# Kernel optimization log

Measured on AMD Instinct MI355X. Metric: run time of the kernel, lower is better.

## Reference

```python
import jax, jax.numpy as jnp
import numpy as np
import math

B, S, HID, H = 1, 2048, 1024, 16
D = HID // H  # head_dim = 64


def setup_inputs() -> dict:
    key = jax.random.key(0)
    ks = jax.random.split(key, 12)
    s = 0.02
    x = jax.random.normal(ks[0], (B, S, HID), jnp.float32)
    Wq = jax.random.normal(ks[1], (HID, HID), jnp.float32) * s
    bq = jnp.zeros((HID,), jnp.float32)
    Wk = jax.random.normal(ks[2], (HID, HID), jnp.float32) * s
    bk = jnp.zeros((HID,), jnp.float32)
    Wv = jax.random.normal(ks[3], (HID, HID), jnp.float32) * s
    bv = jnp.zeros((HID,), jnp.float32)
    Wo = jax.random.normal(ks[4], (HID, HID), jnp.float32) * s
    bo = jnp.zeros((HID,), jnp.float32)
    # nn.Parameter(torch.ones(3,3)) at init; small noise so the bias is non-degenerate
    cmw = jnp.ones((3, 3), jnp.float32) + 0.1 * jax.random.normal(ks[5], (3, 3), jnp.float32)
    # full causal [B,S,S] mask so the mask.shape[1]==seq_len branch is taken
    mask = jnp.tril(jnp.ones((B, S, S), jnp.int32))
    modality_info = jax.random.randint(ks[6], (B, S), 0, 3, dtype=jnp.int64)
    return dict(x=x, Wq=Wq, bq=bq, Wk=Wk, bk=bk, Wv=Wv, bv=bv, Wo=Wo, bo=bo,
                cmw=cmw, mask=mask, modality_info=modality_info)


def reference(x, Wq, bq, Wk, bk, Wv, bv, Wo, bo, cmw, mask, modality_info):
    b, s, _ = x.shape
    # QKV projections (torch Linear: y = x @ W.T + b), split into heads [B,H,S,D]
    q = (x @ Wq.T + bq).reshape(b, s, H, D).transpose(0, 2, 1, 3)
    k = (x @ Wk.T + bk).reshape(b, s, H, D).transpose(0, 2, 1, 3)
    v = (x @ Wv.T + bv).reshape(b, s, H, D).transpose(0, 2, 1, 3)
    scores = jnp.einsum('bhqd,bhkd->bhqk', q, k) / math.sqrt(D)  # [B,H,S,S]
    # cross-modal bias: gather from 3x3 table via pairwise modality indices -> [B,S,S]
    bias = cmw[modality_info[:, :, None], modality_info[:, None, :]]
    scores = scores + bias[:, None, :, :]  # equals original broadcast when B==1
    scores = jnp.where(mask[:, None, :, :] == 0, -1e9, scores)
    attn = jax.nn.softmax(scores, axis=-1)  # dropout is identity in eval
    ctx = jnp.einsum('bhqk,bhkd->bhqd', attn, v)          # [B,H,S,D]
    ctx = ctx.transpose(0, 2, 1, 3).reshape(b, s, HID)    # [B,S,HID]
    return ctx @ Wo.T + bo
```

## Files before the change

### kernel.cpp

```cpp
#include <hip/hip_runtime.h>
#include <hip/hip_bf16.h>
#include <math.h>

#define S_LEN 2048
#define HID   1024
#define NHEAD 16

using bf16x8 = __attribute__((ext_vector_type(8))) short;
using bf16x4 = __attribute__((ext_vector_type(4))) short;
using f32x4  = __attribute__((ext_vector_type(4))) float;

__device__ __forceinline__ float bf2f(short s) {
  union { unsigned u; float f; } c;
  c.u = ((unsigned)(unsigned short)s) << 16;
  return c.f;
}
__device__ __forceinline__ short f2bf(float f) {
  union { float f; unsigned u; } c; c.f = f;
  unsigned u = c.u;
  unsigned r = (u + 0x7fffu + ((u >> 16) & 1u)) >> 16;
  return (short)r;
}
__device__ __forceinline__ float loadf(const void* base, long idx, int is_bf) {
  return is_bf ? bf2f(((const short*)base)[idx]) : ((const float*)base)[idx];
}
__device__ __forceinline__ void gl_lds16(const void* g, void* l) {
  __builtin_amdgcn_global_load_lds(
      (const __attribute__((address_space(1))) void*)g,
      (__attribute__((address_space(3))) void*)l, 16, 0, 0);
}

__global__ void detect_kernel(const unsigned* __restrict__ xw,
                              const int* __restrict__ modw,
                              int* __restrict__ flags) {
  const int t = threadIdx.x;
  int cnt = 0;
  for (int i = t; i < 1024; i += 64) {
    const unsigned fld = (xw[i] >> 7) & 0xFFu;
    cnt += (fld >= 100u && fld <= 135u) ? 1 : 0;
  }
  int odd = 0;
  for (int i = 0; i < 4; ++i) {
    const int wv = modw[2 * (t + 64 * i) + 1];
    odd += (wv != 0) ? 1 : 0;
  }
  for (int m = 1; m < 64; m <<= 1) {
    cnt += __shfl_xor(cnt, m);
    odd += __shfl_xor(odd, m);
  }
  if (t == 0) {
    flags[0] = (cnt >= 512) ? 1 : 0;
    flags[1] = (odd == 0) ? 1 : 0;
  }
}

__global__ __launch_bounds__(256) void convert5(
    const void* __restrict__ s0, const void* __restrict__ s1, const void* __restrict__ s2,
    const void* __restrict__ s3, const void* __restrict__ s4,
    short* __restrict__ d0, short* __restrict__ d1, short* __restrict__ d2,
    short* __restrict__ d3, short* __restrict__ d4,
    const int* __restrict__ flags) {
  const int a = blockIdx.y;
  const void* src = (a == 0) ? s0 : (a == 1) ? s1 : (a == 2) ? s2 : (a == 3) ? s3 : s4;
  short* dst = (a == 0) ? d0 : (a == 1) ? d1 : (a == 2) ? d2 : (a == 3) ? d3 : d4;
  const long n = (a == 0) ? (2L << 20) : (1L << 20);
  const int is_bf = flags[0];
  long i = (long)(blockIdx.x * 256 + threadIdx.x) * 8;
  const long stride = (long)gridDim.x * 256 * 8;
  if (is_bf) {
    for (; i < n; i += stride)
      *(bf16x8*)(dst + i) = *(const bf16x8*)((const short*)src + i);
  } else {
    for (; i < n; i += stride) {
      const float* p = (const float*)src + i;
      bf16x8 r;
#pragma unroll
      for (int j = 0; j < 8; ++j) r[j] = f2bf(p[j]);
      *(bf16x8*)(dst + i) = r;
    }
  }
}

__global__ __launch_bounds__(256) void gemm_bt3(
    const short* __restrict__ A,
    const short* __restrict__ W0, const short* __restrict__ W1, const short* __restrict__ W2,
    const void* __restrict__ b0, const void* __restrict__ b1, const void* __restrict__ b2,
    void* __restrict__ C0, void* __restrict__ C1, void* __restrict__ C2,
    const int* __restrict__ flags, int nbn, int store_f32)
{
  constexpr int K = 1024;
  constexpr int N = 1024;
  __shared__ short As[128 * 32];
  __shared__ short Bs[64 * 32];

  const int t = threadIdx.x;
  const int w = t >> 6, lane = t & 63;
  const int l15 = lane & 15, quad = lane >> 4;
  const int wm = w >> 1, wn = w & 1;
  const int is_bf = flags[0];

  const int mat = blockIdx.x / nbn;
  const int n0 = (blockIdx.x % nbn) * 64;
  const int m0 = blockIdx.y * 128;

  const short* W  = (mat == 0) ? W0 : (mat == 1 ? W1 : W2);
  const void* bia = (mat == 0) ? b0 : (mat == 1 ? b1 : b2);
  void*       C   = (mat == 0) ? C0 : (mat == 1 ? C1 : C2);

  f32x4 acc[4][2];
  for (int mi = 0; mi < 4; ++mi)
    for (int ni = 0; ni < 2; ++ni)
      for (int r = 0; r < 4; ++r) acc[mi][ni][r] = 0.f;

  const int srow = t >> 2;
  const int sch  = (t & 3) * 8;
  const short* Ap = A + (long)(m0 + srow) * K + sch;
  const short* Wp = W + (long)(n0 + srow) * K + sch;
  short* AsW = &As[w * 512];
  short* BsW = &Bs[w * 512];

  for (int kt = 0; kt < K / 32; ++kt) {
    __syncthreads();
    gl_lds16(Ap + kt * 32, AsW);
    gl_lds16(Ap + kt * 32 + 64L * K, AsW + 2048);
    gl_lds16(Wp + kt * 32, BsW);
    __syncthreads();

    bf16x8 af[4], bfr[2];
    for (int mi = 0; mi < 4; ++mi)
      af[mi] = *(const bf16x8*)&As[(wm * 64 + mi * 16 + l15) * 32 + quad * 8];
    for (int ni = 0; ni < 2; ++ni)
      bfr[ni] = *(const bf16x8*)&Bs[(wn * 32 + ni * 16 + l15) * 32 + quad * 8];
    for (int mi = 0; mi < 4; ++mi)
      for (int ni = 0; ni < 2; ++ni)
        acc[mi][ni] = __builtin_amdgcn_mfma_f32_16x16x32_bf16(af[mi], bfr[ni], acc[mi][ni], 0, 0, 0);
  }

  for (int ni = 0; ni < 2; ++ni) {
    const int col = n0 + wn * 32 + ni * 16 + l15;
    const float bv = loadf(bia, col, is_bf);
    for (int mi = 0; mi < 4; ++mi) {
      const int row = m0 + wm * 64 + mi * 16 + quad * 4;
      for (int r = 0; r < 4; ++r) {
        const float v = acc[mi][ni][r] + bv;
        const long idx = (long)(row + r) * N + col;
        if (store_f32) ((float*)C)[idx] = v;
        else           ((short*)C)[idx] = f2bf(v);
      }
    }
  }
}

__global__ __launch_bounds__(256) void attn_split(
    const short* __restrict__ Q, const short* __restrict__ Kg, const short* __restrict__ Vg,
    const int* __restrict__ mod, const void* __restrict__ cmw,
    const int* __restrict__ flags,
    short* __restrict__ PO0, short* __restrict__ PO1,
    float* __restrict__ PL)
{
  __shared__ short Ks[64 * 80];
  __shared__ short Vt[64 * 80];
  __shared__ short Ps[4 * 16 * 80];
  __shared__ float cm[9];
  __shared__ int mods[2048];

  const int t = threadIdx.x;
  const int w = t >> 6, lane = t & 63;
  const int l15 = lane & 15, quad = lane >> 4;
  const int h = blockIdx.y;
  const int pair = blockIdx.x >> 1;
  const int par  = blockIdx.x & 1;
  const int m64 = flags[1];

  if (t < 9) cm[t] = loadf(cmw, t, flags[0]);
  for (int i = t; i < 2048; i += 256) mods[i] = mod[i << m64];
  __syncthreads();

  short* POp = (par == 0) ? PO0 : PO1;
  const int krow = t >> 3, kch = (t & 7) * 8;
  const int vkp = t & 63, vdc = (t >> 6) * 8;

  for (int si = 0; si < 2; ++si) {
    const int strip = (si == 0) ? pair : 31 - pair;
    const int q0 = strip * 64;
    const int nkt = strip + 1;

    const short* qb = Q + (long)(q0 + w * 16 + l15) * HID + h * 64 + quad * 8;
    const bf16x8 aq0 = *(const bf16x8*)qb;
    const bf16x8 aq1 = *(const bf16x8*)(qb + 32);

    int mrow[4];
    for (int r = 0; r < 4; ++r) mrow[r] = mods[q0 + w * 16 + quad * 4 + r];

    float lsum[4];
    f32x4 acc_o[4];
    for (int r = 0; r < 4; ++r) lsum[r] = 0.f;
    for (int ni = 0; ni < 4; ++ni)
      for (int r = 0; r < 4; ++r) acc_o[ni][r] = 0.f;

    bf16x8 rk0, rk1, rv0, rv1;
    if (par < nkt) {
      const long kb = (long)(par * 64) * HID + h * 64;
      rk0 = *(const bf16x8*)(Kg + kb + (long)krow * HID + kch);
      rk1 = *(const bf16x8*)(Kg + kb + (long)(krow + 32) * HID + kch);
      rv0 = *(const bf16x8*)(Vg + kb + (long)vkp * HID + vdc);
      rv1 = *(const bf16x8*)(Vg + kb + (long)vkp * HID + 32 + vdc);
    }

    for (int kt = par; kt < nkt; kt += 2) {
      __syncthreads();
      *(bf16x8*)&Ks[krow * 80 + kch] = rk0;
      *(bf16x8*)&Ks[(krow + 32) * 80 + kch] = rk1;
#pragma unroll
      for (int j = 0; j < 8; ++j) Vt[(vdc + j) * 80 + vkp] = rv0[j];
#pragma unroll
      for (int j = 0; j < 8; ++j) Vt[(vdc + 32 + j) * 80 + vkp] = rv1[j];
      __syncthreads();
      if (kt + 2 < nkt) {
        const long kb = (long)((kt + 2) * 64) * HID + h * 64;
        rk0 = *(const bf16x8*)(Kg + kb + (long)krow * HID + kch);
        rk1 = *(const bf16x8*)(Kg + kb + (long)(krow + 32) * HID + kch);
        rv0 = *(const bf16x8*)(Vg + kb + (long)vkp * HID + vdc);
        rv1 = *(const bf16x8*)(Vg + kb + (long)vkp * HID + 32 + vdc);
      }

      f32x4 sc[4];
      for (int nt = 0; nt < 4; ++nt) {
        const bf16x8 kb0 = *(const bf16x8*)&Ks[(nt * 16 + l15) * 80 + quad * 8];
        const bf16x8 kb1 = *(const bf16x8*)&Ks[(nt * 16 + l15) * 80 + 32 + quad * 8];
        f32x4 z;
        for (int r = 0; r < 4; ++r) z[r] = 0.f;
        z = __builtin_amdgcn_mfma_f32_16x16x32_bf16(aq0, kb0, z, 0, 0, 0);
        z = __builtin_amdgcn_mfma_f32_16x16x32_bf16(aq1, kb1, z, 0, 0, 0);
        sc[nt] = z;
      }

      float sv[4][4];
      for (int nt = 0; nt < 4; ++nt) {
        const int mcol = mods[kt * 64 + nt * 16 + l15];
        for (int r = 0; r < 4; ++r)
          sv[nt][r] = sc[nt][r] * 0.125f + cm[mrow[r] * 3 + mcol];
      }
      if (kt == nkt - 1) {
        for (int nt = 0; nt < 4; ++nt) {
          const int col = kt * 64 + nt * 16 + l15;
          for (int r = 0; r < 4; ++r) {
            const int row = q0 + w * 16 + quad * 4 + r;
            sv[nt][r] = (col <= row) ? sv[nt][r] : -1e30f;
          }
        }
      }
      short pb[4][4];
      for (int nt = 0; nt < 4; ++nt)
        for (int r = 0; r < 4; ++r) {
          const float p = __expf(fminf(sv[nt][r], 60.f));
          lsum[r] += p;
          pb[nt][r] = f2bf(p);
        }

      short* Pw = &Ps[w * 16 * 80];
      for (int nt = 0; nt < 4; ++nt)
        for (int r = 0; r < 4; ++r)
          Pw[(quad * 4 + r) * 80 + nt * 16 + l15] = pb[nt][r];
      asm volatile("s_waitcnt lgkmcnt(0)" ::: "memory");

      for (int kk = 0; kk < 2; ++kk) {
        const bf16x8 ap = *(const bf16x8*)&Pw[l15 * 80 + kk * 32 + quad * 8];
        for (int ni = 0; ni < 4; ++ni) {
          const bf16x8 bv = *(const bf16x8*)&Vt[(ni * 16 + l15) * 80 + kk * 32 + quad * 8];
          acc_o[ni] = __builtin_amdgcn_mfma_f32_16x16x32_bf16(ap, bv, acc_o[ni], 0, 0, 0);
        }
      }
    }

    for (int off = 1; off < 16; off <<= 1)
      for (int r = 0; r < 4; ++r) lsum[r] += __shfl_xor(lsum[r], off);

    for (int ni = 0; ni < 4; ++ni) {
      const int col = h * 64 + ni * 16 + l15;
      for (int r = 0; r < 4; ++r) {
        const int row = q0 + w * 16 + quad * 4 + r;
        POp[(long)row * HID + col] = f2bf(acc_o[ni][r]);
      }
    }
    if (l15 == 0) {
      for (int r = 0; r < 4; ++r) {
        const int row = q0 + w * 16 + quad * 4 + r;
        PL[par * 32768 + row * 16 + h] = lsum[r];
      }
    }
  }
}

__global__ __launch_bounds__(256) void attn_merge(
    const short* __restrict__ PO0, const short* __restrict__ PO1,
    const float* __restrict__ PL, short* __restrict__ CTX)
{
  const int row = blockIdx.x;
  const int t = threadIdx.x;
  const int h = t >> 4;
  const int d0 = (t & 15) * 4;
  const float l0 = PL[row * 16 + h], l1 = PL[32768 + row * 16 + h];
  const float inv = 1.f / (l0 + l1);
  const long b = (long)row * HID + h * 64 + d0;
  const bf16x4 o0 = *(const bf16x4*)&PO0[b];
  const bf16x4 o1 = *(const bf16x4*)&PO1[b];
  bf16x4 out;
#pragma unroll
  for (int j = 0; j < 4; ++j)
    out[j] = f2bf((bf2f(o0[j]) + bf2f(o1[j])) * inv);
  *(bf16x4*)&CTX[b] = out;
}

extern "C" void kernel_launch(void* const* d_in, const int* in_sizes, int n_in,
                              void* d_out, int out_size, void* d_ws, size_t ws_size,
                              hipStream_t stream) {
  constexpr long M1 = 1024L * 1024L;
  int*   flags = (int*)d_ws;
  short* base  = (short*)d_ws + 128;
  short* xb  = base;
  short* Wqb = xb + 2 * M1;
  short* Wkb = Wqb + M1;
  short* Wvb = Wkb + M1;
  short* Wob = Wvb + M1;
  short* Qw  = Wob + M1;
  short* Kw  = Qw + 2 * M1;
  short* Vw  = Kw + 2 * M1;
  short* CTX = Vw + 2 * M1;
  short* PO0 = CTX;
  short* PO1 = xb;
  float* PL  = (float*)Wvb;
  const int* modality = (const int*)d_in[11];

  detect_kernel<<<1, 64, 0, stream>>>((const unsigned*)d_in[0], modality, flags);
  convert5<<<dim3(512, 5), 256, 0, stream>>>(
      d_in[0], d_in[1], d_in[3], d_in[5], d_in[7],
      xb, Wqb, Wkb, Wvb, Wob, flags);

  gemm_bt3<<<dim3(48, 16), 256, 0, stream>>>(
      xb, Wqb, Wkb, Wvb, d_in[2], d_in[4], d_in[6],
      Qw, Kw, Vw, flags, 16, 0);
  attn_split<<<dim3(32, NHEAD), 256, 0, stream>>>(
      Qw, Kw, Vw, modality, d_in[9], flags, PO0, PO1, PL);
  attn_merge<<<dim3(S_LEN), 256, 0, stream>>>(PO0, PO1, PL, CTX);
  gemm_bt3<<<dim3(16, 16), 256, 0, stream>>>(
      CTX, Wob, Wob, Wob, d_in[8], d_in[8], d_in[8],
      d_out, d_out, d_out, flags, 16, 1);
}
```

Measured before the change: 183.2 us.

## Drop detect kernel, convert biases upfront, and double-buffer K/V tiles in attention

Removes the separate single-block detect kernel. Each conversion block now detects the dtype itself, and each attention block detects the int64 modality layout itself, which saves one launch and a serial dependency. Biases and the modality weight table are also converted to bf16 in the same conversion launch, so the GEMM epilogue and attention read them without a dtype branch. The attention inner loop now stages two K/V tiles per barrier pair into double-buffered LDS and prefetches the next two into registers. That halves the barrier count but raises register and LDS use, which may reduce occupancy.

```diff
diff --git a/kernel.cpp b/kernel.cpp
--- a/kernel.cpp
+++ b/kernel.cpp
@@ -21,72 +21,74 @@
   unsigned r = (u + 0x7fffu + ((u >> 16) & 1u)) >> 16;
   return (short)r;
 }
-__device__ __forceinline__ float loadf(const void* base, long idx, int is_bf) {
-  return is_bf ? bf2f(((const short*)base)[idx]) : ((const float*)base)[idx];
-}
 __device__ __forceinline__ void gl_lds16(const void* g, void* l) {
   __builtin_amdgcn_global_load_lds(
       (const __attribute__((address_space(1))) void*)g,
       (__attribute__((address_space(3))) void*)l, 16, 0, 0);
 }
-
-__global__ void detect_kernel(const unsigned* __restrict__ xw,
-                              const int* __restrict__ modw,
-                              int* __restrict__ flags) {
-  const int t = threadIdx.x;
+__device__ __forceinline__ int detect_bf(const unsigned* xw) {
   int cnt = 0;
-  for (int i = t; i < 1024; i += 64) {
+#pragma unroll
+  for (int i = 0; i < 64; ++i) {
     const unsigned fld = (xw[i] >> 7) & 0xFFu;
     cnt += (fld >= 100u && fld <= 135u) ? 1 : 0;
   }
-  int odd = 0;
-  for (int i = 0; i < 4; ++i) {
-    const int wv = modw[2 * (t + 64 * i) + 1];
-    odd += (wv != 0) ? 1 : 0;
-  }
-  for (int m = 1; m < 64; m <<= 1) {
-    cnt += __shfl_xor(cnt, m);
-    odd += __shfl_xor(odd, m);
-  }
-  if (t == 0) {
-    flags[0] = (cnt >= 512) ? 1 : 0;
-    flags[1] = (odd == 0) ? 1 : 0;
-  }
-}
-
-__global__ __launch_bounds__(256) void convert5(
+  return cnt >= 32;
+}
+
+__global__ __launch_bounds__(256) void convert10(
     const void* __restrict__ s0, const void* __restrict__ s1, const void* __restrict__ s2,
-    const void* __restrict__ s3, const void* __restrict__ s4,
+    const void* __restrict__ s3, const void* __restrict__ s4, const void* __restrict__ s5,
+    const void* __restrict__ s6, const void* __restrict__ s7, const void* __restrict__ s8,
+    const void* __restrict__ s9,
     short* __restrict__ d0, short* __restrict__ d1, short* __restrict__ d2,
-    short* __restrict__ d3, short* __restrict__ d4,
-    const int* __restrict__ flags) {
+    short* __restrict__ d3, short* __restrict__ d4, short* __restrict__ d5,
+    short* __restrict__ d6, short* __restrict__ d7, short* __restrict__ d8,
+    short* __restrict__ d9)
+{
+  const int is_bf = detect_bf((const unsigned*)s0);
   const int a = blockIdx.y;
-  const void* src = (a == 0) ? s0 : (a == 1) ? s1 : (a == 2) ? s2 : (a == 3) ? s3 : s4;
-  short* dst = (a == 0) ? d0 : (a == 1) ? d1 : (a == 2) ? d2 : (a == 3) ? d3 : d4;
-  const long n = (a == 0) ? (2L << 20) : (1L << 20);
-  const int is_bf = flags[0];
-  long i = (long)(blockIdx.x * 256 + threadIdx.x) * 8;
-  const long stride = (long)gridDim.x * 256 * 8;
-  if (is_bf) {
+  const void* src; short* dst; long n;
+  if      (a == 0) { src = s0; dst = d0; n = 2L << 20; }
+  else if (a == 1) { src = s1; dst = d1; n = 1L << 20; }
+  else if (a == 2) { src = s2; dst = d2; n = 1L << 20; }
+  else if (a == 3) { src = s3; dst = d3; n = 1L << 20; }
+  else if (a == 4) { src = s4; dst = d4; n = 1L << 20; }
+  else if (a == 5) { src = s5; dst = d5; n = 1024; }
+  else if (a == 6) { src = s6; dst = d6; n = 1024; }
+  else if (a == 7) { src = s7; dst = d7; n = 1024; }
+  else if (a == 8) { src = s8; dst = d8; n = 1024; }
+  else             { src = s9; dst = d9; n = 9; }
+
+  if (n >= 1024) {
+    long i = (long)(blockIdx.x * 256 + threadIdx.x) * 8;
+    const long stride = (long)gridDim.x * 256 * 8;
+    if (is_bf) {
+      for (; i < n; i += stride)
+        *(bf16x8*)(dst + i) = *(const bf16x8*)((const short*)src + i);
+    } else {
+      for (; i < n; i += stride) {
+        const float* p = (const float*)src + i;
+        bf16x8 r;
+#pragma unroll
+        for (int j = 0; j < 8; ++j) r[j] = f2bf(p[j]);
+        *(bf16x8*)(dst + i) = r;
+      }
+    }
+  } else {
+    long i = blockIdx.x * 256 + threadIdx.x;
+    const long stride = (long)gridDim.x * 256;
     for (; i < n; i += stride)
-      *(bf16x8*)(dst + i) = *(const bf16x8*)((const short*)src + i);
-  } else {
-    for (; i < n; i += stride) {
-      const float* p = (const float*)src + i;
-      bf16x8 r;
-#pragma unroll
-      for (int j = 0; j < 8; ++j) r[j] = f2bf(p[j]);
-      *(bf16x8*)(dst + i) = r;
-    }
+      dst[i] = is_bf ? ((const short*)src)[i] : f2bf(((const float*)src)[i]);
   }
 }
 
 __global__ __launch_bounds__(256) void gemm_bt3(
     const short* __restrict__ A,
     const short* __restrict__ W0, const short* __restrict__ W1, const short* __restrict__ W2,
-    const void* __restrict__ b0, const void* __restrict__ b1, const void* __restrict__ b2,
+    const short* __restrict__ b0, const short* __restrict__ b1, const short* __restrict__ b2,
     void* __restrict__ C0, void* __restrict__ C1, void* __restrict__ C2,
-    const int* __restrict__ flags, int nbn, int store_f32)
+    int nbn, int store_f32)
 {
   constexpr int K = 1024;
   constexpr int N = 1024;
@@ -97,14 +99,13 @@
   const int w = t >> 6, lane = t & 63;
   const int l15 = lane & 15, quad = lane >> 4;
   const int wm = w >> 1, wn = w & 1;
-  const int is_bf = flags[0];
 
   const int mat = blockIdx.x / nbn;
   const int n0 = (blockIdx.x % nbn) * 64;
   const int m0 = blockIdx.y * 128;
 
   const short* W  = (mat == 0) ? W0 : (mat == 1 ? W1 : W2);
-  const void* bia = (mat == 0) ? b0 : (mat == 1 ? b1 : b2);
+  const short* bia = (mat == 0) ? b0 : (mat == 1 ? b1 : b2);
   void*       C   = (mat == 0) ? C0 : (mat == 1 ? C1 : C2);
 
   f32x4 acc[4][2];
@@ -138,7 +139,7 @@
 
   for (int ni = 0; ni < 2; ++ni) {
     const int col = n0 + wn * 32 + ni * 16 + l15;
-    const float bv = loadf(bia, col, is_bf);
+    const float bv = bf2f(bia[col]);
     for (int mi = 0; mi < 4; ++mi) {
       const int row = m0 + wm * 64 + mi * 16 + quad * 4;
       for (int r = 0; r < 4; ++r) {
@@ -153,13 +154,12 @@
 
 __global__ __launch_bounds__(256) void attn_split(
     const short* __restrict__ Q, const short* __restrict__ Kg, const short* __restrict__ Vg,
-    const int* __restrict__ mod, const void* __restrict__ cmw,
-    const int* __restrict__ flags,
+    const int* __restrict__ mod, const short* __restrict__ cmw,
     short* __restrict__ PO0, short* __restrict__ PO1,
     float* __restrict__ PL)
 {
-  __shared__ short Ks[64 * 80];
-  __shared__ short Vt[64 * 80];
+  __shared__ short Ks[2][64 * 80];
+  __shared__ short Vt[2][64 * 80];
   __shared__ short Ps[4 * 16 * 80];
   __shared__ float cm[9];
   __shared__ int mods[2048];
@@ -170,13 +170,18 @@
   const int h = blockIdx.y;
   const int pair = blockIdx.x >> 1;
   const int par  = blockIdx.x & 1;
-  const int m64 = flags[1];
-
-  if (t < 9) cm[t] = loadf(cmw, t, flags[0]);
+
+  int oddbits = 0;
+#pragma unroll
+  for (int i = 0; i < 64; ++i) oddbits |= mod[2 * i + 1];
+  const int m64 = (oddbits == 0) ? 1 : 0;
+
+  if (t < 9) cm[t] = bf2f(cmw[t]);
   for (int i = t; i < 2048; i += 256) mods[i] = mod[i << m64];
   __syncthreads();
 
   short* POp = (par == 0) ? PO0 : PO1;
+  short* Pw = &Ps[w * 16 * 80];
   const int krow = t >> 3, kch = (t & 7) * 8;
   const int vkp = t & 63, vdc = (t >> 6) * 8;
 
@@ -198,52 +203,42 @@
     for (int ni = 0; ni < 4; ++ni)
       for (int r = 0; r < 4; ++r) acc_o[ni][r] = 0.f;
 
-    bf16x8 rk0, rk1, rv0, rv1;
-    if (par < nkt) {
-      const long kb = (long)(par * 64) * HID + h * 64;
-      rk0 = *(const bf16x8*)(Kg + kb + (long)krow * HID + kch);
-      rk1 = *(const bf16x8*)(Kg + kb + (long)(krow + 32) * HID + kch);
-      rv0 = *(const bf16x8*)(Vg + kb + (long)vkp * HID + vdc);
-      rv1 = *(const bf16x8*)(Vg + kb + (long)vkp * HID + 32 + vdc);
-    }
-
-    for (int kt = par; kt < nkt; kt += 2) {
-      __syncthreads();
-      *(bf16x8*)&Ks[krow * 80 + kch] = rk0;
-      *(bf16x8*)&Ks[(krow + 32) * 80 + kch] = rk1;
-#pragma unroll
-      for (int j = 0; j < 8; ++j) Vt[(vdc + j) * 80 + vkp] = rv0[j];
-#pragma unroll
-      for (int j = 0; j < 8; ++j) Vt[(vdc + 32 + j) * 80 + vkp] = rv1[j];
-      __syncthreads();
-      if (kt + 2 < nkt) {
-        const long kb = (long)((kt + 2) * 64) * HID + h * 64;
-        rk0 = *(const bf16x8*)(Kg + kb + (long)krow * HID + kch);
-        rk1 = *(const bf16x8*)(Kg + kb + (long)(krow + 32) * HID + kch);
-        rv0 = *(const bf16x8*)(Vg + kb + (long)vkp * HID + vdc);
-        rv1 = *(const bf16x8*)(Vg + kb + (long)vkp * HID + 32 + vdc);
-      }
-
+    bf16x8 rkA[2], rvA[2], rkB[2], rvB[2];
+    auto ldtile = [&](int kt_, bf16x8* rk, bf16x8* rv) {
+      const long kb = (long)(kt_ * 64) * HID + h * 64;
+      rk[0] = *(const bf16x8*)(Kg + kb + (long)krow * HID + kch);
+      rk[1] = *(const bf16x8*)(Kg + kb + (long)(krow + 32) * HID + kch);
+      rv[0] = *(const bf16x8*)(Vg + kb + (long)vkp * HID + vdc);
+      rv[1] = *(const bf16x8*)(Vg + kb + (long)vkp * HID + 32 + vdc);
+    };
+    auto sttile = [&](int buf, bf16x8* rk, bf16x8* rv) {
+      *(bf16x8*)&Ks[buf][krow * 80 + kch] = rk[0];
+      *(bf16x8*)&Ks[buf][(krow + 32) * 80 + kch] = rk[1];
+#pragma unroll
+      for (int j = 0; j < 8; ++j) Vt[buf][(vdc + j) * 80 + vkp] = rv[0][j];
+#pragma unroll
+      for (int j = 0; j < 8; ++j) Vt[buf][(vdc + 32 + j) * 80 + vkp] = rv[1][j];
+    };
+    auto tile_compute = [&](int kt_, int buf) {
       f32x4 sc[4];
       for (int nt = 0; nt < 4; ++nt) {
-        const bf16x8 kb0 = *(const bf16x8*)&Ks[(nt * 16 + l15) * 80 + quad * 8];
-        const bf16x8 kb1 = *(const bf16x8*)&Ks[(nt * 16 + l15) * 80 + 32 + quad * 8];
+        const bf16x8 kb0 = *(const bf16x8*)&Ks[buf][(nt * 16 + l15) * 80 + quad * 8];
+        const bf16x8 kb1 = *(const bf16x8*)&Ks[buf][(nt * 16 + l15) * 80 + 32 + quad * 8];
         f32x4 z;
         for (int r = 0; r < 4; ++r) z[r] = 0.f;
         z = __builtin_amdgcn_mfma_f32_16x16x32_bf16(aq0, kb0, z, 0, 0, 0);
         z = __builtin_amdgcn_mfma_f32_16x16x32_bf16(aq1, kb1, z, 0, 0, 0);
         sc[nt] = z;
       }
-
       float sv[4][4];
       for (int nt = 0; nt < 4; ++nt) {
-        const int mcol = mods[kt * 64 + nt * 16 + l15];
+        const int mcol = mods[kt_ * 64 + nt * 16 + l15];
         for (int r = 0; r < 4; ++r)
           sv[nt][r] = sc[nt][r] * 0.125f + cm[mrow[r] * 3 + mcol];
       }
-      if (kt == nkt - 1) {
+      if (kt_ == nkt - 1) {
         for (int nt = 0; nt < 4; ++nt) {
-          const int col = kt * 64 + nt * 16 + l15;
+          const int col = kt_ * 64 + nt * 16 + l15;
           for (int r = 0; r < 4; ++r) {
             const int row = q0 + w * 16 + quad * 4 + r;
             sv[nt][r] = (col <= row) ? sv[nt][r] : -1e30f;
@@ -257,20 +252,32 @@
           lsum[r] += p;
           pb[nt][r] = f2bf(p);
         }
-
-      short* Pw = &Ps[w * 16 * 80];
       for (int nt = 0; nt < 4; ++nt)
         for (int r = 0; r < 4; ++r)
           Pw[(quad * 4 + r) * 80 + nt * 16 + l15] = pb[nt][r];
       asm volatile("s_waitcnt lgkmcnt(0)" ::: "memory");
-
       for (int kk = 0; kk < 2; ++kk) {
         const bf16x8 ap = *(const bf16x8*)&Pw[l15 * 80 + kk * 32 + quad * 8];
         for (int ni = 0; ni < 4; ++ni) {
-          const bf16x8 bv = *(const bf16x8*)&Vt[(ni * 16 + l15) * 80 + kk * 32 + quad * 8];
+          const bf16x8 bv = *(const bf16x8*)&Vt[buf][(ni * 16 + l15) * 80 + kk * 32 + quad * 8];
           acc_o[ni] = __builtin_amdgcn_mfma_f32_16x16x32_bf16(ap, bv, acc_o[ni], 0, 0, 0);
         }
       }
+    };
+
+    if (par < nkt)     ldtile(par, rkA, rvA);
+    if (par + 2 < nkt) ldtile(par + 2, rkB, rvB);
+
+    for (int kt = par; kt < nkt; kt += 4) {
+      const bool has2 = (kt + 2 < nkt);
+      __syncthreads();
+      sttile(0, rkA, rvA);
+      if (has2) sttile(1, rkB, rvB);
+      __syncthreads();
+      if (kt + 4 < nkt) ldtile(kt + 4, rkA, rvA);
+      if (kt + 6 < nkt) ldtile(kt + 6, rkB, rvB);
+      tile_compute(kt, 0);
+      if (has2) tile_compute(kt + 2, 1);
     }
 
     for (int off = 1; off < 16; off <<= 1)
@@ -316,9 +323,8 @@
                               void* d_out, int out_size, void* d_ws, size_t ws_size,
                               hipStream_t stream) {
   constexpr long M1 = 1024L * 1024L;
-  int*   flags = (int*)d_ws;
-  short* base  = (short*)d_ws + 128;
-  short* xb  = base;
+  short* ws = (short*)d_ws;
+  short* xb  = ws;
   short* Wqb = xb + 2 * M1;
   short* Wkb = Wqb + M1;
   short* Wvb = Wkb + M1;
@@ -327,23 +333,28 @@
   short* Kw  = Qw + 2 * M1;
   short* Vw  = Kw + 2 * M1;
   short* CTX = Vw + 2 * M1;
+  short* bqb = CTX + 2 * M1;
+  short* bkb = bqb + 1024;
+  short* bvb = bkb + 1024;
+  short* bob = bvb + 1024;
+  short* cmb = bob + 1024;
   short* PO0 = CTX;
   short* PO1 = xb;
   float* PL  = (float*)Wvb;
   const int* modality = (const int*)d_in[11];
 
-  detect_kernel<<<1, 64, 0, stream>>>((const unsigned*)d_in[0], modality, flags);
-  convert5<<<dim3(512, 5), 256, 0, stream>>>(
+  convert10<<<dim3(256, 10), 256, 0, stream>>>(
       d_in[0], d_in[1], d_in[3], d_in[5], d_in[7],
-      xb, Wqb, Wkb, Wvb, Wob, flags);
+      d_in[2], d_in[4], d_in[6], d_in[8], d_in[9],
+      xb, Wqb, Wkb, Wvb, Wob, bqb, bkb, bvb, bob, cmb);
 
   gemm_bt3<<<dim3(48, 16), 256, 0, stream>>>(
-      xb, Wqb, Wkb, Wvb, d_in[2], d_in[4], d_in[6],
-      Qw, Kw, Vw, flags, 16, 0);
+      xb, Wqb, Wkb, Wvb, bqb, bkb, bvb,
+      Qw, Kw, Vw, 16, 0);
   attn_split<<<dim3(32, NHEAD), 256, 0, stream>>>(
-      Qw, Kw, Vw, modality, d_in[9], flags, PO0, PO1, PL);
+      Qw, Kw, Vw, modality, cmb, PO0, PO1, PL);
   attn_merge<<<dim3(S_LEN), 256, 0, stream>>>(PO0, PO1, PL, CTX);
   gemm_bt3<<<dim3(16, 16), 256, 0, stream>>>(
-      CTX, Wob, Wob, Wob, d_in[8], d_in[8], d_in[8],
-      d_out, d_out, d_out, flags, 16, 1);
-}
+      CTX, Wob, Wob, Wob, bob, bob, bob,
+      d_out, d_out, d_out, 16, 1);
+}
```

Measured after the change: 183.2 us. About the same (+0.0%).
